# Optimization experiments

Measured on AMD Instinct MI355X. Metric: run time of the kernel, lower is better.

## Reference

```python
import jax, jax.numpy as jnp
import numpy as np

B, T, D = 16, 2048, 256
QK = 64


def setup_inputs() -> dict:
    key = jax.random.key(0)
    ks = jax.random.split(key, 9)
    x = jax.random.normal(ks[0], (B, T, D), dtype=jnp.float32)
    sl = jax.random.uniform(ks[1], (B, T), dtype=jnp.float32)
    mask = jax.random.randint(ks[2], (B, T), 0, 2, dtype=jnp.int32)
    s = 1.0 / np.sqrt(D).astype(np.float32)
    Wq = jax.random.normal(ks[3], (QK, D), dtype=jnp.float32) * s
    bq = jnp.zeros((QK,), dtype=jnp.float32)
    Wk = jax.random.normal(ks[4], (QK, D), dtype=jnp.float32) * s
    bk = jnp.zeros((QK,), dtype=jnp.float32)
    Wv = jax.random.normal(ks[5], (D, D), dtype=jnp.float32) * s
    bv = jnp.zeros((D,), dtype=jnp.float32)
    return {"x": x, "sl": sl, "mask": mask, "Wq": Wq, "bq": bq,
            "Wk": Wk, "bk": bk, "Wv": Wv, "bv": bv}


def reference(x, sl, mask, Wq, bq, Wk, bk, Wv, bv):
    # x: [B,T,D], sl: [B,T] soft labels, mask: [B,T] valid positions
    sl = jnp.clip(sl, 0.0, 1.0)
    q = jnp.einsum('btd,ed->bte', x, Wq) + bq          # [B,T,QK]
    k = jnp.einsum('btd,ed->bte', x, Wk) + bk          # [B,T,QK]
    v = jnp.einsum('btd,ed->bte', x, Wv) + bv          # [B,T,D]
    scale = jnp.float32(1.0 / np.sqrt(QK))
    score = jnp.einsum('bte,bse->bts', q, k) * scale   # [B,T,T]
    # emotion scaling by (1 + sl_j^2) per key position j
    score = score * (1.0 + sl[:, None, :] ** 2)
    score = jnp.where(mask[:, None, :] == 0, jnp.float32(-1e9), score)
    prob = jax.nn.softmax(score, axis=-1)              # [B,T,T]
    out = jnp.einsum('bts,bsd->btd', prob, v)          # [B,T,D]
    return out.mean(axis=1)                            # [B,D]
```

## Files before the change

### kernel.cpp

```cpp
#include <hip/hip_runtime.h>
#include <hip/hip_bf16.h>
#include <stdint.h>

#define B_ 16
#define T_ 2048
#define D_ 256
#define QK_ 64
#define LOG2E 1.44269504088896340736f

typedef _Float16 f16;
typedef _Float16 f16x2 __attribute__((ext_vector_type(2)));
typedef __fp16 fp16x2 __attribute__((ext_vector_type(2)));
typedef _Float16 f16x8 __attribute__((ext_vector_type(8)));
typedef float f32x16 __attribute__((ext_vector_type(16)));

__device__ __forceinline__ void gload_lds16(const void* g, void* l) {
    __builtin_amdgcn_global_load_lds(
        (const __attribute__((address_space(1))) uint32_t*)g,
        (__attribute__((address_space(3))) uint32_t*)l, 16, 0, 0);
}

__device__ __forceinline__ float fexp2(float x) {
#if __has_builtin(__builtin_amdgcn_exp2f)
    return __builtin_amdgcn_exp2f(x);
#else
    return exp2f(x);
#endif
}
__device__ __forceinline__ float flog2(float x) {
#if __has_builtin(__builtin_amdgcn_logf)
    return __builtin_amdgcn_logf(x);
#else
    return log2f(x);
#endif
}
__device__ __forceinline__ f16x2 cvt2(float a, float b) {
#if __has_builtin(__builtin_amdgcn_cvt_pkrtz)
    fp16x2 r = __builtin_amdgcn_cvt_pkrtz(a, b);
    return __builtin_bit_cast(f16x2, r);
#else
    f16x2 r; r[0] = (f16)a; r[1] = (f16)b; return r;
#endif
}
__device__ __forceinline__ f16x8 cvt8(const float* p) {
    union { f16x2 h2[4]; f16x8 h8; } u;
    const float4 a0 = *(const float4*)p;
    const float4 a1 = *(const float4*)(p + 4);
    u.h2[0] = cvt2(a0.x, a0.y); u.h2[1] = cvt2(a0.z, a0.w);
    u.h2[2] = cvt2(a1.x, a1.y); u.h2[3] = cvt2(a1.z, a1.w);
    return u.h8;
}

__global__ __launch_bounds__(256) void proj_mfma(
    const float* __restrict__ x, const float* __restrict__ sl,
    const float* __restrict__ Wq, const float* __restrict__ Wk,
    const float* __restrict__ bq, const float* __restrict__ bk,
    f16* __restrict__ qh, f16* __restrict__ k2h)
{
    __shared__ __align__(16) f16 xs[32 * D_];
    __shared__ float ksc[32];
    const int b = blockIdx.y, t0 = blockIdx.x * 32;
    const int tid = threadIdx.x;
    const int wv = tid >> 6, l = tid & 63, lo = l & 31, hi = l >> 5;

    #pragma unroll
    for (int i = 0; i < 4; ++i) {
        const int f = i * 256 + tid;
        const int r = f >> 5, j = f & 31;
        const f16x8 h = cvt8(x + (size_t)(b * T_ + t0 + r) * D_ + j * 8);
        *(f16x8*)(xs + r * D_ + ((j ^ r) << 3)) = h;
    }
    if (tid < 32) {
        float s = sl[(size_t)b * T_ + t0 + tid];
        s = fminf(fmaxf(s, 0.f), 1.f);
        ksc[tid] = 0.125f * (1.f + s * s) * LOG2E;
    }
    __syncthreads();

    const int c0 = wv * 32;
    const int e = c0 + lo;
    const float* wrow = ((e < 64) ? (Wq + (size_t)e * D_)
                                  : (Wk + (size_t)(e - 64) * D_)) + hi * 8;

    f32x16 acc;
    #pragma unroll
    for (int i = 0; i < 16; ++i) acc[i] = 0.f;

    #pragma unroll
    for (int ks = 0; ks < 16; ++ks) {
        const f16x8 a  = *(const f16x8*)(xs + lo * D_ + ((((ks << 1) + hi) ^ lo) << 3));
        const f16x8 bf = cvt8(wrow + ks * 16);
        acc = __builtin_amdgcn_mfma_f32_32x32x16_f16(a, bf, acc, 0, 0, 0);
    }

    const float bias = (e < 64) ? bq[e] : bk[e - 64];
    __syncthreads();
    f16* hout = xs;
    #pragma unroll
    for (int i = 0; i < 16; ++i) {
        const int row = (i & 3) + 8 * (i >> 2) + 4 * hi;
        float v = acc[i] + bias;
        if (e >= 64) v *= ksc[row];
        hout[row * 128 + e] = (f16)v;
    }
    __syncthreads();
    #pragma unroll
    for (int i = 0; i < 2; ++i) {
        const int f = i * 256 + tid;
        const int rr = f >> 4, j = f & 15;
        const f16x8 v = *(const f16x8*)(hout + rr * 128 + j * 8);
        if (j < 8) *(f16x8*)(qh  + (size_t)(b * T_ + t0 + rr) * QK_ + j * 8) = v;
        else       *(f16x8*)(k2h + (size_t)(b * T_ + t0 + rr) * QK_ + (j - 8) * 8) = v;
    }
}

__global__ __launch_bounds__(256) void z_part(
    const f16* __restrict__ qh, const f16* __restrict__ k2h,
    const int* __restrict__ mask, float* __restrict__ zpart)
{
    __shared__ __align__(16) f16 kt[128 * QK_];
    const int b = blockIdx.y;
    const int t0 = (blockIdx.x & 15) * 128;
    const int ck = blockIdx.x >> 4;
    const int sbase = ck * 128;
    const int tid = threadIdx.x;
    const int wv = tid >> 6, l = tid & 63, lo = l & 31, hi = l >> 5;

    {
        const char* src = (const char*)(k2h + (size_t)(b * T_ + sbase) * QK_);
        #pragma unroll
        for (int i = 0; i < 4; ++i) {
            const int o = wv * 4096 + i * 1024 + l * 16;
            const int r = o >> 7, jc = (o >> 4) & 7;
            gload_lds16(src + r * 128 + ((jc ^ (r & 7)) << 4),
                        (char*)kt + wv * 4096 + i * 1024);
        }
    }

    const f16* qrow = qh + (size_t)(b * T_ + t0 + wv * 32 + lo) * QK_ + hi * 8;
    f16x8 a[4];
    #pragma unroll
    for (int kc = 0; kc < 4; ++kc) a[kc] = *(const f16x8*)(qrow + kc * 16);

    float zp[16];
    #pragma unroll
    for (int i = 0; i < 16; ++i) zp[i] = 0.f;

    __syncthreads();

    #pragma unroll
    for (int cg = 0; cg < 4; ++cg) {
        const int srow = cg * 32 + lo;
        const float mb = mask[b * T_ + sbase + srow] ? 0.f : -1e9f;
        f32x16 c;
        #pragma unroll
        for (int i = 0; i < 16; ++i) c[i] = mb;
        #pragma unroll
        for (int kc = 0; kc < 4; ++kc) {
            const int jcc = (kc * 2 + hi) ^ (srow & 7);
            const f16x8 bf = *(const f16x8*)((const char*)kt + srow * 128 + (jcc << 4));
            c = __builtin_amdgcn_mfma_f32_32x32x16_f16(a[kc], bf, c, 0, 0, 0);
        }
        #pragma unroll
        for (int i = 0; i < 16; ++i) zp[i] += fexp2(c[i]);
    }

    #pragma unroll
    for (int off = 1; off <= 16; off <<= 1)
        #pragma unroll
        for (int i = 0; i < 16; ++i) zp[i] += __shfl_xor(zp[i], off);

    if (lo == 0) {
        #pragma unroll
        for (int i = 0; i < 16; ++i) {
            const int row = (i & 3) + 8 * (i >> 2) + 4 * hi;
            zpart[(size_t)(b * 16 + ck) * T_ + t0 + wv * 32 + row] = zp[i];
        }
    }
}

__global__ __launch_bounds__(256) void w_part(
    const f16* __restrict__ qh, const f16* __restrict__ k2h,
    const float* __restrict__ zpart, float* __restrict__ wpart)
{
    __shared__ __align__(16) f16 qt[128 * QK_];
    __shared__ float lz_s[128];
    const int b = blockIdx.y;
    const int s0b = (blockIdx.x & 15) * 128;
    const int tc = blockIdx.x >> 4;
    const int tbase = tc * 128;
    const int tid = threadIdx.x;
    const int wv = tid >> 6, l = tid & 63, lo = l & 31, hi = l >> 5;

    {
        const char* src = (const char*)(qh + (size_t)(b * T_ + tbase) * QK_);
        #pragma unroll
        for (int i = 0; i < 4; ++i) {
            const int o = wv * 4096 + i * 1024 + l * 16;
            const int r = o >> 7, jc = (o >> 4) & 7;
            gload_lds16(src + r * 128 + ((jc ^ (r & 7)) << 4),
                        (char*)qt + wv * 4096 + i * 1024);
        }
    }
    if (tid < 128) {
        const float* zb = zpart + (size_t)(b * 16) * T_ + tbase + tid;
        float z = 0.f;
        #pragma unroll
        for (int ckk = 0; ckk < 16; ++ckk) z += zb[(size_t)ckk * T_];
        lz_s[tid] = -flog2(z);
    }

    const f16* krow = k2h + (size_t)(b * T_ + s0b + wv * 32 + lo) * QK_ + hi * 8;
    f16x8 a[4];
    #pragma unroll
    for (int kc = 0; kc < 4; ++kc) a[kc] = *(const f16x8*)(krow + kc * 16);

    float wp[16];
    #pragma unroll
    for (int i = 0; i < 16; ++i) wp[i] = 0.f;

    __syncthreads();

    #pragma unroll
    for (int cg = 0; cg < 4; ++cg) {
        const int trow = cg * 32 + lo;
        const float bias = lz_s[trow];
        f32x16 c;
        #pragma unroll
        for (int i = 0; i < 16; ++i) c[i] = bias;
        #pragma unroll
        for (int kc = 0; kc < 4; ++kc) {
            const int jcc = (kc * 2 + hi) ^ (trow & 7);
            const f16x8 bf = *(const f16x8*)((const char*)qt + trow * 128 + (jcc << 4));
            c = __builtin_amdgcn_mfma_f32_32x32x16_f16(a[kc], bf, c, 0, 0, 0);
        }
        #pragma unroll
        for (int i = 0; i < 16; ++i) wp[i] += fexp2(c[i]);
    }

    #pragma unroll
    for (int off = 1; off <= 16; off <<= 1)
        #pragma unroll
        for (int i = 0; i < 16; ++i) wp[i] += __shfl_xor(wp[i], off);

    if (lo == 0) {
        #pragma unroll
        for (int i = 0; i < 16; ++i) {
            const int row = (i & 3) + 8 * (i >> 2) + 4 * hi;
            wpart[(size_t)(b * 16 + tc) * T_ + s0b + wv * 32 + row] = wp[i];
        }
    }
}

__global__ __launch_bounds__(256) void y_fused(
    const float* __restrict__ x, const float* __restrict__ wpart,
    const int* __restrict__ mask, float* __restrict__ ypart,
    float* __restrict__ swp)
{
    __shared__ float wloc[32];
    const int b  = blockIdx.y;
    const int ch = blockIdx.x;
    const int tid = threadIdx.x;

    if (tid < 32) {
        const int s = ch * 32 + tid;
        const float* wb = wpart + (size_t)(b * 16) * T_ + s;
        float v = 0.f;
        #pragma unroll
        for (int ckk = 0; ckk < 16; ++ckk) v += wb[(size_t)ckk * T_];
        v *= mask[b * T_ + s] ? (1.f / (float)T_) : 0.f;
        wloc[tid] = v;
        float sv = v;
        #pragma unroll
        for (int off = 1; off <= 16; off <<= 1) sv += __shfl_xor(sv, off);
        if (tid == 0) swp[b * 64 + ch] = sv;
    }
    __syncthreads();

    const int d = tid;
    const float* xb = x + ((size_t)b * T_ + ch * 32) * D_;
    float acc = 0.f;
    #pragma unroll 8
    for (int s = 0; s < 32; ++s) acc += wloc[s] * xb[(size_t)s * D_ + d];
    ypart[((size_t)b * 64 + ch) * D_ + d] = acc;
}

__global__ __launch_bounds__(256) void outkernel(
    const float* __restrict__ ypart, const float* __restrict__ swp,
    const float* __restrict__ Wv, const float* __restrict__ bv,
    float* __restrict__ out)
{
    __shared__ __align__(16) float ys[D_];
    __shared__ float sw0;
    const int b   = blockIdx.x;
    const int tid = threadIdx.x;

    float yv = 0.f;
    #pragma unroll
    for (int ch = 0; ch < 64; ++ch) yv += ypart[((size_t)b * 64 + ch) * D_ + tid];
    ys[tid] = yv;

    float s = (tid < 64) ? swp[b * 64 + tid] : 0.f;
    #pragma unroll
    for (int off = 1; off <= 32; off <<= 1) s += __shfl_xor(s, off);
    if (tid == 0) sw0 = s;
    __syncthreads();

    const float sw = sw0;
    const float4* wv4 = (const float4*)(Wv + (size_t)tid * D_);
    const float4* ys4 = (const float4*)ys;
    float o = 0.f;
    for (int i = 0; i < D_ / 4; ++i) {
        const float4 a = wv4[i];
        const float4 y = ys4[i];
        o += a.x * y.x + a.y * y.y + a.z * y.z + a.w * y.w;
    }
    out[(size_t)b * D_ + tid] = o + bv[tid] * sw;
}

extern "C" void kernel_launch(void* const* d_in, const int* in_sizes, int n_in,
                              void* d_out, int out_size, void* d_ws, size_t ws_size,
                              hipStream_t stream)
{
    const float* x    = (const float*)d_in[0];
    const float* sl   = (const float*)d_in[1];
    const int*   mask = (const int*)d_in[2];
    const float* Wq   = (const float*)d_in[3];
    const float* bq   = (const float*)d_in[4];
    const float* Wk   = (const float*)d_in[5];
    const float* bk   = (const float*)d_in[6];
    const float* Wv   = (const float*)d_in[7];
    const float* bv   = (const float*)d_in[8];
    float* out = (float*)d_out;

    f16*   qh    = (f16*)d_ws;
    f16*   k2h   = qh + (size_t)B_ * T_ * QK_;
    float* zpart = (float*)(k2h + (size_t)B_ * T_ * QK_);
    float* wpart = zpart + (size_t)B_ * 16 * T_;
    float* swp   = wpart + (size_t)B_ * 16 * T_;
    float* yp    = swp + B_ * 64;

    proj_mfma<<<dim3(T_ / 32, B_), 256, 0, stream>>>(x, sl, Wq, Wk, bq, bk, qh, k2h);
    z_part   <<<dim3(256, B_), 256, 0, stream>>>(qh, k2h, mask, zpart);
    w_part   <<<dim3(256, B_), 256, 0, stream>>>(qh, k2h, zpart, wpart);
    y_fused  <<<dim3(64, B_), 256, 0, stream>>>(x, wpart, mask, yp, swp);
    outkernel<<<dim3(B_), 256, 0, stream>>>(yp, swp, Wv, bv, out);
}
```

Before: 90.37 us.

## Store MFMA-fragment-ordered Q/K copies and reduce row sums through LDS

```diff
diff --git a/kernel.cpp b/kernel.cpp
--- a/kernel.cpp
+++ b/kernel.cpp
@@ -55,11 +55,12 @@
     const float* __restrict__ x, const float* __restrict__ sl,
     const float* __restrict__ Wq, const float* __restrict__ Wk,
     const float* __restrict__ bq, const float* __restrict__ bk,
-    f16* __restrict__ qh, f16* __restrict__ k2h)
+    f16* __restrict__ qh, f16* __restrict__ k2h,
+    f16* __restrict__ qf, f16* __restrict__ kf)
 {
     __shared__ __align__(16) f16 xs[32 * D_];
     __shared__ float ksc[32];
-    const int b = blockIdx.y, t0 = blockIdx.x * 32;
+    const int b = blockIdx.y, tile = blockIdx.x, t0 = tile * 32;
     const int tid = threadIdx.x;
     const int wv = tid >> 6, l = tid & 63, lo = l & 31, hi = l >> 5;
 
@@ -112,17 +113,23 @@
         if (j < 8) *(f16x8*)(qh  + (size_t)(b * T_ + t0 + rr) * QK_ + j * 8) = v;
         else       *(f16x8*)(k2h + (size_t)(b * T_ + t0 + rr) * QK_ + (j - 8) * 8) = v;
     }
+    {
+        const int kc2 = tid >> 6, hi2 = (tid >> 5) & 1, lo2 = tid & 31;
+        const f16* srcq = hout + lo2 * 128 + kc2 * 16 + hi2 * 8;
+        const size_t tb = ((size_t)b * 64 + tile) * 2048 + tid * 8;
+        *(f16x8*)(qf + tb) = *(const f16x8*)srcq;
+        *(f16x8*)(kf + tb) = *(const f16x8*)(srcq + 64);
+    }
 }
 
 __global__ __launch_bounds__(256) void z_part(
-    const f16* __restrict__ qh, const f16* __restrict__ k2h,
+    const f16* __restrict__ qf, const f16* __restrict__ k2h,
     const int* __restrict__ mask, float* __restrict__ zpart)
 {
     __shared__ __align__(16) f16 kt[128 * QK_];
     const int b = blockIdx.y;
-    const int t0 = (blockIdx.x & 15) * 128;
-    const int ck = blockIdx.x >> 4;
-    const int sbase = ck * 128;
+    const int tIdx = blockIdx.x & 15, t0 = tIdx * 128;
+    const int ck = blockIdx.x >> 4,  sbase = ck * 128;
     const int tid = threadIdx.x;
     const int wv = tid >> 6, l = tid & 63, lo = l & 31, hi = l >> 5;
 
@@ -137,10 +144,10 @@
         }
     }
 
-    const f16* qrow = qh + (size_t)(b * T_ + t0 + wv * 32 + lo) * QK_ + hi * 8;
+    const f16* abase = qf + ((size_t)b * 64 + tIdx * 4 + wv) * 2048 + l * 8;
     f16x8 a[4];
     #pragma unroll
-    for (int kc = 0; kc < 4; ++kc) a[kc] = *(const f16x8*)(qrow + kc * 16);
+    for (int kc = 0; kc < 4; ++kc) a[kc] = *(const f16x8*)(abase + kc * 512);
 
     float zp[16];
     #pragma unroll
@@ -165,30 +172,35 @@
         for (int i = 0; i < 16; ++i) zp[i] += fexp2(c[i]);
     }
 
-    #pragma unroll
-    for (int off = 1; off <= 16; off <<= 1)
-        #pragma unroll
-        for (int i = 0; i < 16; ++i) zp[i] += __shfl_xor(zp[i], off);
-
-    if (lo == 0) {
-        #pragma unroll
-        for (int i = 0; i < 16; ++i) {
-            const int row = (i & 3) + 8 * (i >> 2) + 4 * hi;
-            zpart[(size_t)(b * 16 + ck) * T_ + t0 + wv * 32 + row] = zp[i];
-        }
+    __syncthreads();
+    float* red = (float*)kt;
+    #pragma unroll
+    for (int i = 0; i < 16; ++i) {
+        const int row = wv * 32 + (i & 3) + 8 * (i >> 2) + 4 * hi;
+        const int col = (lo & 3) | ((((lo >> 2) ^ row) & 7) << 2);
+        red[row * 32 + col] = zp[i];
+    }
+    __syncthreads();
+    if (tid < 128) {
+        float s = 0.f;
+        #pragma unroll
+        for (int c = 0; c < 8; ++c) {
+            const float4 v = *(const float4*)(red + tid * 32 + (((c ^ tid) & 7) << 2));
+            s += v.x + v.y + v.z + v.w;
+        }
+        zpart[(size_t)(b * 16 + ck) * T_ + t0 + tid] = s;
     }
 }
 
 __global__ __launch_bounds__(256) void w_part(
-    const f16* __restrict__ qh, const f16* __restrict__ k2h,
+    const f16* __restrict__ kf, const f16* __restrict__ qh,
     const float* __restrict__ zpart, float* __restrict__ wpart)
 {
     __shared__ __align__(16) f16 qt[128 * QK_];
     __shared__ float lz_s[128];
     const int b = blockIdx.y;
-    const int s0b = (blockIdx.x & 15) * 128;
-    const int tc = blockIdx.x >> 4;
-    const int tbase = tc * 128;
+    const int sIdx = blockIdx.x & 15, s0b = sIdx * 128;
+    const int tc = blockIdx.x >> 4,  tbase = tc * 128;
     const int tid = threadIdx.x;
     const int wv = tid >> 6, l = tid & 63, lo = l & 31, hi = l >> 5;
 
@@ -210,10 +222,10 @@
         lz_s[tid] = -flog2(z);
     }
 
-    const f16* krow = k2h + (size_t)(b * T_ + s0b + wv * 32 + lo) * QK_ + hi * 8;
+    const f16* abase = kf + ((size_t)b * 64 + sIdx * 4 + wv) * 2048 + l * 8;
     f16x8 a[4];
     #pragma unroll
-    for (int kc = 0; kc < 4; ++kc) a[kc] = *(const f16x8*)(krow + kc * 16);
+    for (int kc = 0; kc < 4; ++kc) a[kc] = *(const f16x8*)(abase + kc * 512);
 
     float wp[16];
     #pragma unroll
@@ -238,17 +250,23 @@
         for (int i = 0; i < 16; ++i) wp[i] += fexp2(c[i]);
     }
 
-    #pragma unroll
-    for (int off = 1; off <= 16; off <<= 1)
-        #pragma unroll
-        for (int i = 0; i < 16; ++i) wp[i] += __shfl_xor(wp[i], off);
-
-    if (lo == 0) {
-        #pragma unroll
-        for (int i = 0; i < 16; ++i) {
-            const int row = (i & 3) + 8 * (i >> 2) + 4 * hi;
-            wpart[(size_t)(b * 16 + tc) * T_ + s0b + wv * 32 + row] = wp[i];
-        }
+    __syncthreads();
+    float* red = (float*)qt;
+    #pragma unroll
+    for (int i = 0; i < 16; ++i) {
+        const int row = wv * 32 + (i & 3) + 8 * (i >> 2) + 4 * hi;
+        const int col = (lo & 3) | ((((lo >> 2) ^ row) & 7) << 2);
+        red[row * 32 + col] = wp[i];
+    }
+    __syncthreads();
+    if (tid < 128) {
+        float s = 0.f;
+        #pragma unroll
+        for (int c = 0; c < 8; ++c) {
+            const float4 v = *(const float4*)(red + tid * 32 + (((c ^ tid) & 7) << 2));
+            s += v.x + v.y + v.z + v.w;
+        }
+        wpart[(size_t)(b * 16 + tc) * T_ + s0b + tid] = s;
     }
 }
 
@@ -334,15 +352,17 @@
     float* out = (float*)d_out;
 
     f16*   qh    = (f16*)d_ws;
-    f16*   k2h   = qh + (size_t)B_ * T_ * QK_;
-    float* zpart = (float*)(k2h + (size_t)B_ * T_ * QK_);
+    f16*   k2h   = qh  + (size_t)B_ * T_ * QK_;
+    f16*   qf    = k2h + (size_t)B_ * T_ * QK_;
+    f16*   kf    = qf  + (size_t)B_ * T_ * QK_;
+    float* zpart = (float*)(kf + (size_t)B_ * T_ * QK_);
     float* wpart = zpart + (size_t)B_ * 16 * T_;
     float* swp   = wpart + (size_t)B_ * 16 * T_;
     float* yp    = swp + B_ * 64;
 
-    proj_mfma<<<dim3(T_ / 32, B_), 256, 0, stream>>>(x, sl, Wq, Wk, bq, bk, qh, k2h);
-    z_part   <<<dim3(256, B_), 256, 0, stream>>>(qh, k2h, mask, zpart);
-    w_part   <<<dim3(256, B_), 256, 0, stream>>>(qh, k2h, zpart, wpart);
+    proj_mfma<<<dim3(T_ / 32, B_), 256, 0, stream>>>(x, sl, Wq, Wk, bq, bk, qh, k2h, qf, kf);
+    z_part   <<<dim3(256, B_), 256, 0, stream>>>(qf, k2h, mask, zpart);
+    w_part   <<<dim3(256, B_), 256, 0, stream>>>(kf, qh, zpart, wpart);
     y_fused  <<<dim3(64, B_), 256, 0, stream>>>(x, wpart, mask, yp, swp);
     outkernel<<<dim3(B_), 256, 0, stream>>>(yp, swp, Wv, bv, out);
 }
```

New measurement: 82.60 us. 1.09x faster.
